# Kernel tuning notes

Hardware: AMD Instinct MI355X
Metric: run time of the kernel (lower is better)

The kernel has to match this reference:

```python
import jax, jax.numpy as jnp
import numpy as np

B, N, K, C_IN, C_OUT = 4, 8192, 16, 128, 128


def setup_inputs() -> dict:
    key = jax.random.key(0)
    k1, k2, k3 = jax.random.split(key, 3)
    x = jax.random.normal(k1, (B, N, C_IN), dtype=jnp.float32)
    edge_index = jax.random.randint(k2, (2, B, N, K), 0, N, dtype=jnp.int64)
    W = jax.random.normal(k3, (C_OUT, C_IN), dtype=jnp.float32) * (1.0 / np.sqrt(C_IN))
    b = jnp.zeros((C_OUT,), dtype=jnp.float32)
    eps = jnp.zeros((1,), dtype=jnp.float32)  # eps_init = 0.0
    return {"x": x, "edge_index": edge_index, "W": W, "b": b, "eps": eps}


def reference(x, edge_index, W, b, eps):
    # x: [B, N, C], edge_index: [2, B, N, K] -- use source index edge_index[0]
    idx = edge_index[0]                                   # [B, N, K]
    # gather neighbor features per batch: x_j[b,n,k,:] = x[b, idx[b,n,k], :]
    x_j = jax.vmap(lambda xb, ib: xb[ib])(x, idx)         # [B, N, K, C]
    agg = jnp.sum(x_j, axis=2)                            # sum over neighbors -> [B, N, C]
    h = (1.0 + eps) * x + agg                             # eps-scaled residual
    # MLP([in, out], act='relu'): single linear + relu on channel dim
    out = jax.nn.relu(jnp.einsum("bnc,oc->bno", h, W) + b)
    return out
```

## Files before the change

kernel.cpp:

```cpp
#include <hip/hip_runtime.h>
#include <stdint.h>

#define BATCH   4
#define NNODE   8192
#define KNBR    16
#define CIN     128
#define COUT    128
#define MB      32
#define THREADS 256
#define HS_STRIDE 136

#define XELEM   (BATCH * NNODE * CIN)
#define WELEM   (COUT * CIN)
#define CVT_XBLK (XELEM / (256 * 8))
#define CVT_WBLK (WELEM / (256 * 8))

typedef __attribute__((ext_vector_type(8))) short short8;
typedef __attribute__((ext_vector_type(4))) float f32x4;
typedef __attribute__((ext_vector_type(4))) int   i32x4;

__device__ __forceinline__ short bf16_rne(float f) {
    union { float f; uint32_t u; } v; v.f = f;
    return (short)((v.u + 0x7FFFu + ((v.u >> 16) & 1u)) >> 16);
}
__device__ __forceinline__ float bf16_f32(short s) {
    union { uint32_t u; float f; } v; v.u = ((uint32_t)(uint16_t)s) << 16;
    return v.f;
}

__global__ __launch_bounds__(256)
void cvt_bf16(const float* __restrict__ x, const float* __restrict__ W,
              ushort* __restrict__ xb) {
    const int bi = blockIdx.x;
    const float* src;
    ushort*      dst;
    int          gid;
    if (bi < CVT_XBLK) { src = x; dst = xb;          gid = bi * 256 + threadIdx.x; }
    else               { src = W; dst = xb + XELEM;  gid = (bi - CVT_XBLK) * 256 + threadIdx.x; }
    const f32x4* xp = (const f32x4*)src + (size_t)gid * 2;
    f32x4 a = __builtin_nontemporal_load(xp);
    f32x4 c = __builtin_nontemporal_load(xp + 1);
    short8 s;
    s[0]=bf16_rne(a[0]); s[1]=bf16_rne(a[1]); s[2]=bf16_rne(a[2]); s[3]=bf16_rne(a[3]);
    s[4]=bf16_rne(c[0]); s[5]=bf16_rne(c[1]); s[6]=bf16_rne(c[2]); s[7]=bf16_rne(c[3]);
    ((short8*)dst)[gid] = s;
}

template<bool USEBF>
__global__ __launch_bounds__(THREADS, 2)
void gin_fused(const float*  __restrict__ x,
               const ushort* __restrict__ xb,
               const ushort* __restrict__ wb,
               const int*    __restrict__ eidx,
               const float*  __restrict__ W,
               const float*  __restrict__ bias,
               const float*  __restrict__ epsp,
               float*        __restrict__ out)
{
    __shared__ __align__(16) short h_s[MB * HS_STRIDE];

    const int tid = threadIdx.x;
    const int i   = blockIdx.x;
    const int xcd = i & 7;
    const int sub = i >> 3;
    const int b   = xcd >> 1;
    const int wbi = ((xcd & 1) << 7) | sub;
    const int n0  = wbi * MB;
    const int row0 = b * NNODE + n0;

    const float eps1 = 1.0f + epsp[0];

    {
        const int r  = tid >> 3;
        const int q  = tid & 7;
        const int n  = n0 + r;
        const int c0 = q * 16;
        const int* ip = eidx + ((size_t)b * NNODE + n) * KNBR;

        int js[KNBR];
        #pragma unroll
        for (int p = 0; p < 4; ++p) {
            i32x4 jv = __builtin_nontemporal_load((const i32x4*)(ip + p * 4));
            js[p*4+0]=jv.x; js[p*4+1]=jv.y; js[p*4+2]=jv.z; js[p*4+3]=jv.w;
        }

        float acc[16];

        if constexpr (USEBF) {
            const ushort* xbb = xb + (size_t)b * NNODE * CIN;
            const ushort* xs  = xbb + (size_t)n * CIN + c0;
            short8 s0 = *(const short8*)xs, s1 = *(const short8*)(xs + 8);

            short8 t0[KNBR], t1[KNBR];
            #pragma unroll
            for (int k = 0; k < KNBR; ++k) {
                const ushort* xn = xbb + (size_t)js[k] * CIN + c0;
                t0[k] = *(const short8*)xn;
                t1[k] = *(const short8*)(xn + 8);
            }

            #pragma unroll
            for (int e = 0; e < 8; ++e) {
                acc[e]     = eps1 * bf16_f32(s0[e]);
                acc[8 + e] = eps1 * bf16_f32(s1[e]);
            }
            #pragma unroll
            for (int k = 0; k < KNBR; ++k) {
                #pragma unroll
                for (int e = 0; e < 8; ++e) {
                    acc[e]     += bf16_f32(t0[k][e]);
                    acc[8 + e] += bf16_f32(t1[k][e]);
                }
            }
        } else {
            const float* xbb = x + (size_t)b * NNODE * CIN;
            const float* xs  = xbb + (size_t)n * CIN + c0;
            #pragma unroll
            for (int p = 0; p < 4; ++p) {
                f32x4 v = *(const f32x4*)(xs + p * 4);
                acc[p*4+0]=eps1*v[0]; acc[p*4+1]=eps1*v[1]; acc[p*4+2]=eps1*v[2]; acc[p*4+3]=eps1*v[3];
            }
            #pragma unroll
            for (int k = 0; k < KNBR; ++k) {
                const float* xn = xbb + (size_t)js[k] * CIN + c0;
                #pragma unroll
                for (int p = 0; p < 4; ++p) {
                    f32x4 v = *(const f32x4*)(xn + p * 4);
                    acc[p*4+0]+=v[0]; acc[p*4+1]+=v[1]; acc[p*4+2]+=v[2]; acc[p*4+3]+=v[3];
                }
            }
        }

        short* hp = h_s + r * HS_STRIDE + c0;
        #pragma unroll
        for (int p = 0; p < 2; ++p) {
            short8 s;
            #pragma unroll
            for (int e = 0; e < 8; ++e) s[e] = bf16_rne(acc[p*8+e]);
            *(short8*)(hp + p * 8) = s;
        }
    }

    const int wave = tid >> 6;
    const int lane = tid & 63;
    const int l16  = lane & 15;
    const int lq   = lane >> 4;

    short8 bfrag[2][4];
    if constexpr (USEBF) {
        #pragma unroll
        for (int t = 0; t < 2; ++t) {
            const ushort* wp = wb + (size_t)(wave * 32 + t * 16 + l16) * CIN;
            #pragma unroll
            for (int kb = 0; kb < 4; ++kb)
                bfrag[t][kb] = *(const short8*)(wp + kb * 32 + lq * 8);
        }
    } else {
        #pragma unroll
        for (int t = 0; t < 2; ++t) {
            const float* wp = W + (size_t)(wave * 32 + t * 16 + l16) * CIN;
            #pragma unroll
            for (int kb = 0; kb < 4; ++kb) {
                const float* wq = wp + kb * 32 + lq * 8;
                f32x4 f0 = *(const f32x4*)(wq);
                f32x4 f1 = *(const f32x4*)(wq + 4);
                short8 s;
                s[0]=bf16_rne(f0[0]); s[1]=bf16_rne(f0[1]); s[2]=bf16_rne(f0[2]); s[3]=bf16_rne(f0[3]);
                s[4]=bf16_rne(f1[0]); s[5]=bf16_rne(f1[1]); s[6]=bf16_rne(f1[2]); s[7]=bf16_rne(f1[3]);
                bfrag[t][kb] = s;
            }
        }
    }
    const float bias0 = bias[wave * 32 + l16];
    const float bias1 = bias[wave * 32 + 16 + l16];

    __syncthreads();

    float* outb = out + (size_t)row0 * COUT;
    #pragma unroll
    for (int rt = 0; rt < MB / 16; ++rt) {
        const short* ap = h_s + (rt * 16 + l16) * HS_STRIDE + lq * 8;
        short8 afrag[4];
        #pragma unroll
        for (int kb = 0; kb < 4; ++kb)
            afrag[kb] = *(const short8*)(ap + kb * 32);

        #pragma unroll
        for (int t = 0; t < 2; ++t) {
            f32x4 acc = { 0.f, 0.f, 0.f, 0.f };
            #pragma unroll
            for (int kb = 0; kb < 4; ++kb)
                acc = __builtin_amdgcn_mfma_f32_16x16x32_bf16(afrag[kb], bfrag[t][kb], acc, 0, 0, 0);

            const float bv  = t ? bias1 : bias0;
            const int   col = wave * 32 + t * 16 + l16;
            #pragma unroll
            for (int ii = 0; ii < 4; ++ii) {
                const int row = rt * 16 + lq * 4 + ii;
                float v = acc[ii] + bv;
                v = v > 0.f ? v : 0.f;
                __builtin_nontemporal_store(v, &outb[(size_t)row * COUT + col]);
            }
        }
    }
}

extern "C" void kernel_launch(void* const* d_in, const int* in_sizes, int n_in,
                              void* d_out, int out_size, void* d_ws, size_t ws_size,
                              hipStream_t stream) {
    const float* x    = (const float*)d_in[0];
    const int*   eidx = (const int*)d_in[1];
    const float* W    = (const float*)d_in[2];
    const float* bias = (const float*)d_in[3];
    const float* eps  = (const float*)d_in[4];
    float*       out  = (float*)d_out;

    const size_t need = (size_t)(XELEM + WELEM) * sizeof(ushort);
    dim3 grid((BATCH * NNODE) / MB);

    if (ws_size >= need) {
        ushort* xb = (ushort*)d_ws;
        cvt_bf16<<<dim3(CVT_XBLK + CVT_WBLK), dim3(256), 0, stream>>>(x, W, xb);
        gin_fused<true><<<grid, dim3(THREADS), 0, stream>>>(x, xb, xb + XELEM, eidx, W, bias, eps, out);
    } else {
        gin_fused<false><<<grid, dim3(THREADS), 0, stream>>>(x, nullptr, nullptr, eidx, W, bias, eps, out);
    }
}
```

Baseline: 94.96 us.

## Remap neighbor gather so each wave reads whole bf16 rows coalesced

Changes the bf16 gather-sum so that each wave processes 8 nodes and each lane loads a 4-byte pair of channels from every neighbor row. A wave's loads then cover one full 256-byte row per neighbor instead of scattered 32-byte pieces. This aims to improve memory coalescing and cache-line use for the random-neighbor gather, at the cost of many more, narrower load instructions and a large register array of in-flight loads. The fp32 fallback path is untouched apart from dropping a nontemporal hint on index loads.

```diff
diff --git a/kernel.cpp b/kernel.cpp
--- a/kernel.cpp
+++ b/kernel.cpp
@@ -26,6 +26,12 @@
 __device__ __forceinline__ float bf16_f32(short s) {
     union { uint32_t u; float f; } v; v.u = ((uint32_t)(uint16_t)s) << 16;
     return v.f;
+}
+__device__ __forceinline__ float bf16_lo(uint32_t u) {
+    union { uint32_t u; float f; } v; v.u = u << 16;  return v.f;
+}
+__device__ __forceinline__ float bf16_hi(uint32_t u) {
+    union { uint32_t u; float f; } v; v.u = u & 0xFFFF0000u; return v.f;
 }
 
 __global__ __launch_bounds__(256)
@@ -70,7 +76,43 @@
 
     const float eps1 = 1.0f + epsp[0];
 
-    {
+    if constexpr (USEBF) {
+        const int wv = tid >> 6;
+        const int ln = tid & 63;
+        const ushort* xbb = xb + (size_t)b * NNODE * CIN;
+
+        uint32_t t[8][KNBR];
+        #pragma unroll
+        for (int rr = 0; rr < 8; ++rr) {
+            const int n = n0 + wv * 8 + rr;
+            const int* ip = eidx + ((size_t)b * NNODE + n) * KNBR;
+            int js[KNBR];
+            #pragma unroll
+            for (int p = 0; p < 4; ++p) {
+                i32x4 jv = __builtin_nontemporal_load((const i32x4*)(ip + p * 4));
+                js[p*4+0]=jv.x; js[p*4+1]=jv.y; js[p*4+2]=jv.z; js[p*4+3]=jv.w;
+            }
+            #pragma unroll
+            for (int k = 0; k < KNBR; ++k)
+                t[rr][k] = *(const uint32_t*)(xbb + (size_t)js[k] * CIN + ln * 2);
+        }
+
+        #pragma unroll
+        for (int rr = 0; rr < 8; ++rr) {
+            const int n = n0 + wv * 8 + rr;
+            uint32_t own = *(const uint32_t*)(xbb + (size_t)n * CIN + ln * 2);
+            float lo = eps1 * bf16_lo(own);
+            float hi = eps1 * bf16_hi(own);
+            #pragma unroll
+            for (int k = 0; k < KNBR; ++k) {
+                lo += bf16_lo(t[rr][k]);
+                hi += bf16_hi(t[rr][k]);
+            }
+            uint32_t packed = (uint32_t)(uint16_t)bf16_rne(lo)
+                            | ((uint32_t)(uint16_t)bf16_rne(hi) << 16);
+            *(uint32_t*)(h_s + (size_t)(wv * 8 + rr) * HS_STRIDE + ln * 2) = packed;
+        }
+    } else {
         const int r  = tid >> 3;
         const int q  = tid & 7;
         const int n  = n0 + r;
@@ -80,57 +122,26 @@
         int js[KNBR];
         #pragma unroll
         for (int p = 0; p < 4; ++p) {
-            i32x4 jv = __builtin_nontemporal_load((const i32x4*)(ip + p * 4));
+            i32x4 jv = *(const i32x4*)(ip + p * 4);
             js[p*4+0]=jv.x; js[p*4+1]=jv.y; js[p*4+2]=jv.z; js[p*4+3]=jv.w;
         }
-
         float acc[16];
-
-        if constexpr (USEBF) {
-            const ushort* xbb = xb + (size_t)b * NNODE * CIN;
-            const ushort* xs  = xbb + (size_t)n * CIN + c0;
-            short8 s0 = *(const short8*)xs, s1 = *(const short8*)(xs + 8);
-
-            short8 t0[KNBR], t1[KNBR];
-            #pragma unroll
-            for (int k = 0; k < KNBR; ++k) {
-                const ushort* xn = xbb + (size_t)js[k] * CIN + c0;
-                t0[k] = *(const short8*)xn;
-                t1[k] = *(const short8*)(xn + 8);
-            }
-
-            #pragma unroll
-            for (int e = 0; e < 8; ++e) {
-                acc[e]     = eps1 * bf16_f32(s0[e]);
-                acc[8 + e] = eps1 * bf16_f32(s1[e]);
-            }
-            #pragma unroll
-            for (int k = 0; k < KNBR; ++k) {
-                #pragma unroll
-                for (int e = 0; e < 8; ++e) {
-                    acc[e]     += bf16_f32(t0[k][e]);
-                    acc[8 + e] += bf16_f32(t1[k][e]);
-                }
-            }
-        } else {
-            const float* xbb = x + (size_t)b * NNODE * CIN;
-            const float* xs  = xbb + (size_t)n * CIN + c0;
+        const float* xbb = x + (size_t)b * NNODE * CIN;
+        const float* xs  = xbb + (size_t)n * CIN + c0;
+        #pragma unroll
+        for (int p = 0; p < 4; ++p) {
+            f32x4 v = *(const f32x4*)(xs + p * 4);
+            acc[p*4+0]=eps1*v[0]; acc[p*4+1]=eps1*v[1]; acc[p*4+2]=eps1*v[2]; acc[p*4+3]=eps1*v[3];
+        }
+        #pragma unroll
+        for (int k = 0; k < KNBR; ++k) {
+            const float* xn = xbb + (size_t)js[k] * CIN + c0;
             #pragma unroll
             for (int p = 0; p < 4; ++p) {
-                f32x4 v = *(const f32x4*)(xs + p * 4);
-                acc[p*4+0]=eps1*v[0]; acc[p*4+1]=eps1*v[1]; acc[p*4+2]=eps1*v[2]; acc[p*4+3]=eps1*v[3];
-            }
-            #pragma unroll
-            for (int k = 0; k < KNBR; ++k) {
-                const float* xn = xbb + (size_t)js[k] * CIN + c0;
-                #pragma unroll
-                for (int p = 0; p < 4; ++p) {
-                    f32x4 v = *(const f32x4*)(xn + p * 4);
-                    acc[p*4+0]+=v[0]; acc[p*4+1]+=v[1]; acc[p*4+2]+=v[2]; acc[p*4+3]+=v[3];
-                }
-            }
-        }
-
+                f32x4 v = *(const f32x4*)(xn + p * 4);
+                acc[p*4+0]+=v[0]; acc[p*4+1]+=v[1]; acc[p*4+2]+=v[2]; acc[p*4+3]+=v[3];
+            }
+        }
         short* hp = h_s + r * HS_STRIDE + c0;
         #pragma unroll
         for (int p = 0; p < 2; ++p) {
```

New measurement: 100.2 us. 1.05x slower.
